# Performance work log

Hardware: AMD Instinct MI355X
Metric: run time of the kernel (lower is better)

The kernel has to match this reference:

```python
import jax, jax.numpy as jnp
import numpy as np

N, E, IN_DIM, HID, HEADS = 50000, 800000, 160, 64, 4
NEG_SLOPE = 0.2
BN_EPS = 1e-5


def setup_inputs() -> dict:
    key = jax.random.key(0)
    ks = jax.random.split(key, 32)
    s = lambda i, shape, sc=0.05: jax.random.normal(ks[i], shape, dtype=jnp.float32) * sc
    inp = {
        "x": jax.random.normal(ks[0], (N, IN_DIM), dtype=jnp.float32),
        "edge_index": jax.random.randint(ks[1], (2, E), 0, N, dtype=jnp.int64),
        # conv1: GATv2Conv(160 -> 64, heads=4, concat=True)
        "Wl1": s(2, (IN_DIM, HEADS * HID)), "bl1": s(3, (HEADS * HID,)),
        "Wr1": s(4, (IN_DIM, HEADS * HID)), "br1": s(5, (HEADS * HID,)),
        "att1": s(6, (HEADS, HID)), "bias1": s(7, (HEADS * HID,)),
        # bn1 (eval mode)
        "g1": jnp.ones((HEADS * HID,), jnp.float32), "b1": s(8, (HEADS * HID,)),
        "m1": s(9, (HEADS * HID,)), "v1": jax.random.uniform(ks[10], (HEADS * HID,), jnp.float32, 0.5, 1.5),
        # conv2: GATv2Conv(256 -> 64, heads=1, concat=False)
        "Wl2": s(11, (HEADS * HID, HID)), "bl2": s(12, (HID,)),
        "Wr2": s(13, (HEADS * HID, HID)), "br2": s(14, (HID,)),
        "att2": s(15, (1, HID)), "bias2": s(16, (HID,)),
        # bn2 (eval mode)
        "g2": jnp.ones((HID,), jnp.float32), "b2": s(17, (HID,)),
        "m2": s(18, (HID,)), "v2": jax.random.uniform(ks[19], (HID,), jnp.float32, 0.5, 1.5),
        # skip and output linear
        "Ws": s(20, (IN_DIM, HID)), "bs": s(21, (HID,)),
        "Wo": s(22, (HID, 1)), "bo": s(23, (1,)),
    }
    return inp


def gatv2_conv(x, Wl, bl, Wr, br, att, bias, src, dst, heads, out_dim, concat):
    n = x.shape[0]
    xl = (x @ Wl + bl).reshape(n, heads, out_dim)   # source transform
    xr = (x @ Wr + br).reshape(n, heads, out_dim)   # target transform
    e = jax.nn.leaky_relu(xl[src] + xr[dst], NEG_SLOPE)       # [E', H, D]
    logits = jnp.einsum('ehd,hd->eh', e, att)                 # [E', H]
    # segment softmax over incoming edges per target node
    mx = jax.ops.segment_max(logits, dst, num_segments=n)     # [N, H]
    a = jnp.exp(logits - mx[dst])
    denom = jax.ops.segment_sum(a, dst, num_segments=n)
    alpha = a / denom[dst]                                    # [E', H]
    out = jax.ops.segment_sum(xl[src] * alpha[:, :, None], dst, num_segments=n)  # [N, H, D]
    out = out.reshape(n, heads * out_dim) if concat else out.mean(axis=1)
    return out + bias


def reference(x, edge_index, Wl1, bl1, Wr1, br1, att1, bias1, g1, b1, m1, v1,
              Wl2, bl2, Wr2, br2, att2, bias2, g2, b2, m2, v2, Ws, bs, Wo, bo):
    n = x.shape[0]
    loop = jnp.arange(n, dtype=edge_index.dtype)
    src = jnp.concatenate([edge_index[0], loop])   # PyG add_self_loops=True
    dst = jnp.concatenate([edge_index[1], loop])

    x_skip = x @ Ws + bs
    h = gatv2_conv(x, Wl1, bl1, Wr1, br1, att1, bias1, src, dst, HEADS, HID, True)
    h = jax.nn.relu((h - m1) * g1 / jnp.sqrt(v1 + BN_EPS) + b1)  # BN1 eval + relu
    h = gatv2_conv(h, Wl2, bl2, Wr2, br2, att2, bias2, src, dst, 1, HID, False)
    h = jax.nn.relu((h - m2) * g2 / jnp.sqrt(v2 + BN_EPS) + b2)  # BN2 eval + relu
    h = h + x_skip
    return (h @ Wo + bo).squeeze(-1)               # [N]
```

## Files before the change

kernel.cpp:

```cpp
#include <hip/hip_runtime.h>
#include <hip/hip_bf16.h>

#define N_NODES 50000
#define E_EDGES 800000
#define EP_EDGES 850000
#define IN_DIM 160
#define HEADS 4
#define HID 64
#define C1 256
#define NEG_SLOPE 0.2f
#define BN_EPS 1e-5f

typedef __attribute__((ext_vector_type(8))) short bf16x8;
typedef __attribute__((ext_vector_type(4))) float f32x4;
typedef _Float16 h2 __attribute__((ext_vector_type(2)));

__device__ __forceinline__ float b2f(ushort u) {
    return __uint_as_float(((unsigned)u) << 16);
}
__device__ __forceinline__ ushort f2b(float f) {
    __hip_bfloat16 h = __float2bfloat16(f);
    return *reinterpret_cast<ushort*>(&h);
}
__device__ __forceinline__ ushort f2h(float f) {
    union { _Float16 h; ushort u; } c;
    c.h = (_Float16)f;
    return c.u;
}
__device__ __forceinline__ float lo16(uint u) { return __uint_as_float(u << 16); }
__device__ __forceinline__ float hi16(uint u) { return __uint_as_float(u & 0xffff0000u); }
__device__ __forceinline__ h2 uh(uint u) {
    union { uint u; h2 h; } c; c.u = u; return c.h;
}

__device__ __forceinline__ bool probe_f32(const ushort* xraw) {
    int lane = threadIdx.x & 63;
    float a = fabsf(b2f(xraw[2 * lane]));
    unsigned long long m = __ballot(a > 1e-6f && a < 1e6f);
    return __popcll(m) < 48;
}
__device__ __forceinline__ bool probe_i64(const int* eraw) {
    int lane = threadIdx.x & 63;
    unsigned long long m = __ballot(eraw[2 * lane + 1] != 0);
    return __popcll(m) < 8;
}

template<int CTRL>
__device__ __forceinline__ float dpp_add(float p) {
    int t = __builtin_amdgcn_update_dpp(0, __float_as_int(p), CTRL, 0xf, 0xf, true);
    return p + __int_as_float(t);
}
__device__ __forceinline__ float row16_sum(float p) {
    p = dpp_add<0xB1>(p);
    p = dpp_add<0x4E>(p);
    p = dpp_add<0x124>(p);
    p = dpp_add<0x128>(p);
    return p;
}

#define NB_SWZ 62
#define NB_HIST 3321

struct SW2 {
    const void* W[5];
    ushort* D[5];
    ushort* U;
    int NT[5];
    int base[5];
    const void* sp[19];
    const void* xraw;
};

__global__ void front_k(const int* __restrict__ ei, int* __restrict__ deg,
                        int* __restrict__ epos, SW2 s, ushort* __restrict__ params) {
    const int b = blockIdx.x;
    if (b < NB_SWZ) {
        const bool f32 = probe_f32((const ushort*)s.xraw);
        if (b < 61) {
            int idx = b * 256 + threadIdx.x;
            int seg = 0;
            #pragma unroll
            for (int k = 1; k < 5; ++k) seg += (idx >= s.base[k]) ? 1 : 0;
            int li = idx - s.base[seg];
            int NT = s.NT[seg];
            int N = NT << 4;
            int lane = li & 63;
            int ft = li >> 6;
            int kb = ft / NT, t = ft - kb * NT;
            int q = lane >> 4, m = lane & 15;
            const float* pf = (const float*)s.W[seg];
            const ushort* pu = (const ushort*)s.W[seg];
            ushort* d;
            if (seg < 3) {
                const int FO = (seg == 0) ? 0 : (seg == 1) ? 16 : 32;
                d = s.U + ((size_t)(kb * 36 + FO + t) * 64 + lane) * 8;
            } else {
                d = s.D[seg] + (size_t)li * 8;
            }
            #pragma unroll
            for (int j = 0; j < 8; ++j) {
                size_t src = (size_t)(kb * 32 + q * 8 + j) * N + t * 16 + m;
                d[j] = f32 ? f2b(pf[src]) : pu[src];
            }
        } else {
            const int SZ[19] = {256,256,256,256,256,256,256,256,
                                64,64,64,64,64,64,64,64,64,64, 1};
            const int OF[19] = {40960,82176,82432,82688,82944,83200,83456,83712,
                                100352,116800,116864,116928,116992,117056,117120,117184,
                                127488,127552, 127616};
            for (int e = threadIdx.x; e < 2689; e += 256) {
                int rem = e, t = 0;
                while (rem >= SZ[t]) { rem -= SZ[t]; ++t; }
                const float* pf = (const float*)s.sp[t];
                const ushort* pu = (const ushort*)s.sp[t];
                float val = f32 ? pf[rem] : b2f(pu[rem]);
                params[OF[t] + rem] = (t == 2 || t == 10) ? f2h(val) : f2b(val);
            }
        }
    } else {
        const bool i64 = probe_i64(ei);
        int e = (b - NB_SWZ) * 256 + threadIdx.x;
        if (e >= EP_EDGES) return;
        int dst;
        if (e < E_EDGES) {
            int idx = E_EDGES + e;
            dst = i64 ? ei[2 * idx] : ei[idx];
        } else dst = e - E_EDGES;
        epos[e] = atomicAdd(&deg[dst], 1);
    }
}

__global__ __launch_bounds__(1024) void scan1_k(const int* __restrict__ deg,
                                                int* __restrict__ exc,
                                                int* __restrict__ bsum) {
    __shared__ int wsum[16];
    const int t = threadIdx.x;
    const int lane = t & 63, w = t >> 6;
    int i = blockIdx.x * 1024 + t;
    int v = (i < N_NODES) ? deg[i] : 0;
    int sIncl = v;
    #pragma unroll
    for (int d = 1; d < 64; d <<= 1) {
        int u = __shfl_up(sIncl, d);
        if (lane >= d) sIncl += u;
    }
    if (lane == 63) wsum[w] = sIncl;
    __syncthreads();
    if (w == 0) {
        int p = (lane < 16) ? wsum[lane] : 0;
        #pragma unroll
        for (int d = 1; d < 16; d <<= 1) {
            int u = __shfl_up(p, d);
            if (lane >= d) p += u;
        }
        if (lane < 16) wsum[lane] = p;
    }
    __syncthreads();
    int base = (w > 0) ? wsum[w - 1] : 0;
    int incl = base + sIncl;
    if (i < N_NODES) exc[i] = incl - v;
    if (t == 1023) bsum[blockIdx.x] = incl;
}

__global__ void scan2_k(const int* __restrict__ bsum, int* __restrict__ cp,
                        int* __restrict__ exc) {
    int lane = threadIdx.x;
    int v = (lane < 49) ? bsum[lane] : 0;
    int orig = v;
    #pragma unroll
    for (int d = 1; d < 64; d <<= 1) {
        int u = __shfl_up(v, d);
        if (lane >= d) v += u;
    }
    if (lane < 49) cp[lane] = v - orig;
    if (lane == 48) exc[N_NODES] = EP_EDGES - (v - orig);
}

__device__ __forceinline__ bf16x8 loadA(const void* X, bool f32, size_t row, int off) {
    if (!f32) return *(const bf16x8*)((const ushort*)X + row * IN_DIM + off);
    const float* p = (const float*)X + row * IN_DIM + off;
    bf16x8 r;
    #pragma unroll
    for (int j = 0; j < 8; ++j) r[j] = (short)f2b(p[j]);
    return r;
}

#define NB_G3 3128

__global__ __launch_bounds__(256, 4) void scatgemm_k(const void* __restrict__ A,
                                                     const ushort* __restrict__ U,
                                                     const ushort* __restrict__ bi1,
                                                     const ushort* __restrict__ bi2,
                                                     const ushort* __restrict__ bi3,
                                                     ushort* __restrict__ o1,
                                                     ushort* __restrict__ o2,
                                                     ushort* __restrict__ o3,
                                                     int M,
                                                     const int* __restrict__ ei,
                                                     const int* __restrict__ epos,
                                                     const int* __restrict__ exc,
                                                     const int* __restrict__ cp,
                                                     int* __restrict__ col) {
    if (blockIdx.x >= NB_G3) {
        const bool i64 = probe_i64(ei);
        int e = (blockIdx.x - NB_G3) * 256 + threadIdx.x;
        if (e >= EP_EDGES) return;
        int src, dst;
        if (e < E_EDGES) {
            if (i64) { src = ei[2 * e]; dst = ei[2 * (E_EDGES + e)]; }
            else     { src = ei[e];     dst = ei[E_EDGES + e]; }
        } else { src = e - E_EDGES; dst = src; }
        col[exc[dst] + cp[dst >> 10] + epos[e]] = src;
        return;
    }
    const bool f32 = probe_f32((const ushort*)A);
    const int wave = threadIdx.x >> 6;
    const int lane = threadIdx.x & 63;
    const int cg = blockIdx.x & 3;
    const int rb = blockIdx.x >> 2;
    const int row0 = rb * 64 + wave * 16;
    if (row0 >= M) return;
    const int ar = row0 + (lane & 15);
    const int aoff = (lane >> 4) * 8;
    const bf16x8* bu = (const bf16x8*)U;
    f32x4 acc[9] = {};
    #pragma unroll
    for (int kb = 0; kb < 5; ++kb) {
        bf16x8 af = loadA(A, f32, (size_t)ar, aoff + kb * 32);
        #pragma unroll
        for (int jj = 0; jj < 9; ++jj) {
            bf16x8 b = bu[(size_t)(kb * 36 + cg * 9 + jj) * 64 + lane];
            acc[jj] = __builtin_amdgcn_mfma_f32_16x16x32_bf16(af, b, acc[jj], 0, 0, 0);
        }
    }
    const int cn = lane & 15, cq = lane >> 4;
    #pragma unroll
    for (int jj = 0; jj < 9; ++jj) {
        const int f = cg * 9 + jj;
        ushort* op; int ldc, colb; const ushort* bp_; bool tobf;
        if (f < 16)      { op = o1; ldc = C1;  colb = f * 16;        bp_ = bi1 + f * 16;        tobf = false; }
        else if (f < 32) { op = o2; ldc = C1;  colb = (f - 16) * 16; bp_ = bi2 + (f - 16) * 16; tobf = false; }
        else             { op = o3; ldc = HID; colb = (f - 32) * 16; bp_ = bi3 + (f - 32) * 16; tobf = true;  }
        const float bb = b2f(bp_[cn]);
        #pragma unroll
        for (int r = 0; r < 4; ++r) {
            const int grow = row0 + cq * 4 + r;
            const float v = acc[jj][r] + bb;
            op[(size_t)grow * ldc + colb + cn] = tobf ? f2b(v) : f2h(v);
        }
    }
}

__global__ __launch_bounds__(256) void gemm2_k(const ushort* __restrict__ A,
                                               const ushort* __restrict__ B1,
                                               const ushort* __restrict__ B2,
                                               const ushort* __restrict__ bi1,
                                               const ushort* __restrict__ bi2,
                                               ushort* __restrict__ o1,
                                               ushort* __restrict__ o2,
                                               int M) {
    const int wave = threadIdx.x >> 6;
    const int lane = threadIdx.x & 63;
    const int row0 = blockIdx.x * 64 + wave * 16;
    if (row0 >= M) return;
    int arow = row0 + (lane & 15);
    if (arow >= M) arow = M - 1;
    const ushort* aptr = A + (size_t)arow * C1 + (lane >> 4) * 8;
    const bf16x8* b1 = (const bf16x8*)B1;
    const bf16x8* b2 = (const bf16x8*)B2;
    f32x4 aL[4] = {}, aR[4] = {};
    #pragma unroll
    for (int kb = 0; kb < 8; ++kb) {
        bf16x8 af = *(const bf16x8*)(aptr + kb * 32);
        #pragma unroll
        for (int t = 0; t < 4; ++t)
            aL[t] = __builtin_amdgcn_mfma_f32_16x16x32_bf16(af, b1[(kb * 4 + t) * 64 + lane], aL[t], 0, 0, 0);
        #pragma unroll
        for (int t = 0; t < 4; ++t)
            aR[t] = __builtin_amdgcn_mfma_f32_16x16x32_bf16(af, b2[(kb * 4 + t) * 64 + lane], aR[t], 0, 0, 0);
    }
    const int cn = lane & 15, cq = lane >> 4;
    #pragma unroll
    for (int t = 0; t < 4; ++t) {
        float bbL = b2f(bi1[t * 16 + cn]);
        float bbR = b2f(bi2[t * 16 + cn]);
        #pragma unroll
        for (int r = 0; r < 4; ++r) {
            int grow = row0 + cq * 4 + r;
            if (grow < M) {
                o1[(size_t)grow * HID + t * 16 + cn] = f2h(aL[t][r] + bbL);
                o2[(size_t)grow * HID + t * 16 + cn] = f2h(aR[t][r] + bbR);
            }
        }
    }
}

__global__ __launch_bounds__(256) void conv1_k(const ushort* __restrict__ xl,
                                               const ushort* __restrict__ xr,
                                               const int* __restrict__ exc,
                                               const int* __restrict__ cp,
                                               const int* __restrict__ col,
                                               const ushort* __restrict__ att,
                                               const ushort* __restrict__ bias1,
                                               const ushort* __restrict__ g1,
                                               const ushort* __restrict__ b1,
                                               const ushort* __restrict__ m1,
                                               const ushort* __restrict__ v1,
                                               ushort* __restrict__ h1out) {
    const int n = blockIdx.x * 4 + (threadIdx.x >> 6);
    if (n >= N_NODES) return;
    const int lane = threadIdx.x & 63;
    const int g = lane >> 4;
    const int r = lane & 15;
    const uint4* xr4 = (const uint4*)(xr + (size_t)n * C1 + r * 16);
    const uint4 xru0 = xr4[0], xru1 = xr4[1];
    const uint4* at4 = (const uint4*)(att + r * 16);
    const uint4 atu0 = at4[0], atu1 = at4[1];
    h2 xrp[8], atp[8];
    xrp[0] = uh(xru0.x); xrp[1] = uh(xru0.y); xrp[2] = uh(xru0.z); xrp[3] = uh(xru0.w);
    xrp[4] = uh(xru1.x); xrp[5] = uh(xru1.y); xrp[6] = uh(xru1.z); xrp[7] = uh(xru1.w);
    atp[0] = uh(atu0.x); atp[1] = uh(atu0.y); atp[2] = uh(atu0.z); atp[3] = uh(atu0.w);
    atp[4] = uh(atu1.x); atp[5] = uh(atu1.y); atp[6] = uh(atu1.z); atp[7] = uh(atu1.w);
    const h2 ns2 = {(_Float16)NEG_SLOPE, (_Float16)NEG_SLOPE};
    const int e0 = exc[n] + cp[n >> 10];
    const int e1 = exc[n + 1] + cp[(n + 1) >> 10];
    float a[16];
    #pragma unroll
    for (int k = 0; k < 16; ++k) a[k] = 0.f;
    float den = 0.f;
    int j = e0 + g;

    auto body = [&](uint4 u0, uint4 u1, bool masked, int jm) {
        h2 xp[8];
        xp[0] = uh(u0.x); xp[1] = uh(u0.y); xp[2] = uh(u0.z); xp[3] = uh(u0.w);
        xp[4] = uh(u1.x); xp[5] = uh(u1.y); xp[6] = uh(u1.z); xp[7] = uh(u1.w);
        h2 d0 = {(_Float16)0, (_Float16)0};
        h2 d1 = {(_Float16)0, (_Float16)0};
        #pragma unroll
        for (int k = 0; k < 8; k += 2) {
            h2 t0 = xp[k] + xrp[k];
            t0 = __builtin_elementwise_max(t0, t0 * ns2);
            d0 = __builtin_elementwise_fma(t0, atp[k], d0);
            h2 t1 = xp[k + 1] + xrp[k + 1];
            t1 = __builtin_elementwise_max(t1, t1 * ns2);
            d1 = __builtin_elementwise_fma(t1, atp[k + 1], d1);
        }
        h2 ds = d0 + d1;
        float p = (float)ds.x + (float)ds.y;
        p = dpp_add<0xB1>(p);
        p = dpp_add<0x4E>(p);
        float w = __expf(fminf(p, 60.f));
        if (masked) w = (jm < e1) ? w : 0.f;
        den += w;
        #pragma unroll
        for (int k = 0; k < 8; ++k) {
            a[2 * k]     = fmaf(w, (float)xp[k].x, a[2 * k]);
            a[2 * k + 1] = fmaf(w, (float)xp[k].y, a[2 * k + 1]);
        }
    };
    auto rowp = [&](int s) { return (const uint4*)(xl + (size_t)(uint)s * C1 + r * 16); };

    int sA = col[j < e1 ? j : e1 - 1];
    int sB = col[j + 4 < e1 ? j + 4 : e1 - 1];
    int i = e0;
    for (; i + 8 <= e1; i += 8) {
        const int jn = i + g + 8;
        int sC = col[jn < e1 ? jn : e1 - 1];
        int sD = col[jn + 4 < e1 ? jn + 4 : e1 - 1];
        const uint4* pA = rowp(sA);
        uint4 a0 = pA[0], a1 = pA[1];
        const uint4* pB = rowp(sB);
        uint4 b0 = pB[0], b1v = pB[1];
        body(a0, a1, false, 0);
        body(b0, b1v, false, 0);
        sA = sC; sB = sD;
    }
    j = i + g;
    if (i + 4 <= e1) {
        const uint4* pA = rowp(sA);
        uint4 a0 = pA[0], a1 = pA[1];
        body(a0, a1, false, 0);
        sA = sB; i += 4; j += 4;
    }
    if (j < e1) {
        const uint4* pA = rowp(sA);
        uint4 a0 = pA[0], a1 = pA[1];
        body(a0, a1, true, j);
    }

    #pragma unroll
    for (int k = 0; k < 16; ++k) {
        a[k] += __shfl_xor(a[k], 16);
        a[k] += __shfl_xor(a[k], 32);
    }
    den += __shfl_xor(den, 16);
    den += __shfl_xor(den, 32);
    const int q = g;
    float s0 = q == 0 ? a[0] : q == 1 ? a[4] : q == 2 ? a[8]  : a[12];
    float s1 = q == 0 ? a[1] : q == 1 ? a[5] : q == 2 ? a[9]  : a[13];
    float s2 = q == 0 ? a[2] : q == 1 ? a[6] : q == 2 ? a[10] : a[14];
    float s3 = q == 0 ? a[3] : q == 1 ? a[7] : q == 2 ? a[11] : a[15];
    const int pi = r * 4 + q;
    const float inv = 1.f / den;
    const uint2 biu = ((const uint2*)bias1)[pi];
    const uint2 gu  = ((const uint2*)g1)[pi];
    const uint2 bu  = ((const uint2*)b1)[pi];
    const uint2 mu  = ((const uint2*)m1)[pi];
    const uint2 vu  = ((const uint2*)v1)[pi];
    float o0 = fmaf(s0, inv, lo16(biu.x));
    float o1 = fmaf(s1, inv, hi16(biu.x));
    float o2 = fmaf(s2, inv, lo16(biu.y));
    float o3 = fmaf(s3, inv, hi16(biu.y));
    float c0 = lo16(gu.x) * rsqrtf(lo16(vu.x) + BN_EPS);
    float c1 = hi16(gu.x) * rsqrtf(hi16(vu.x) + BN_EPS);
    float c2 = lo16(gu.y) * rsqrtf(lo16(vu.y) + BN_EPS);
    float c3 = hi16(gu.y) * rsqrtf(hi16(vu.y) + BN_EPS);
    float h0 = fmaxf((o0 - lo16(mu.x)) * c0 + lo16(bu.x), 0.f);
    float h1v = fmaxf((o1 - hi16(mu.x)) * c1 + hi16(bu.x), 0.f);
    float h2v = fmaxf((o2 - lo16(mu.y)) * c2 + lo16(bu.y), 0.f);
    float h3 = fmaxf((o3 - hi16(mu.y)) * c3 + hi16(bu.y), 0.f);
    uint2 ou;
    ou.x = (uint)f2b(h0) | ((uint)f2b(h1v) << 16);
    ou.y = (uint)f2b(h2v) | ((uint)f2b(h3) << 16);
    ((uint2*)h1out)[(size_t)n * 64 + pi] = ou;
}

__global__ __launch_bounds__(256) void conv2_k(const ushort* __restrict__ xl,
                                               const ushort* __restrict__ xr,
                                               const ushort* __restrict__ xskip,
                                               const int* __restrict__ exc,
                                               const int* __restrict__ cp,
                                               const int* __restrict__ col,
                                               const ushort* __restrict__ att2,
                                               const ushort* __restrict__ bias2,
                                               const ushort* __restrict__ g2,
                                               const ushort* __restrict__ bb2,
                                               const ushort* __restrict__ m2,
                                               const ushort* __restrict__ v2,
                                               const ushort* __restrict__ Wo,
                                               const ushort* __restrict__ bo,
                                               void* __restrict__ out,
                                               const ushort* __restrict__ xraw) {
    const bool f32out = probe_f32(xraw);
    const int n = blockIdx.x * 4 + (threadIdx.x >> 6);
    if (n >= N_NODES) return;
    const int lane = threadIdx.x & 63;
    const int grp = lane >> 4;
    const uint m = lane & 15;
    const uint2* xl2v = (const uint2*)xl;
    const uint2 xru = ((const uint2*)xr)[(size_t)n * 16 + m];
    const h2 xr01 = uh(xru.x), xr23 = uh(xru.y);
    const uint2 atu = ((const uint2*)att2)[m];
    const h2 at01 = uh(atu.x), at23 = uh(atu.y);
    const h2 ns2 = {(_Float16)NEG_SLOPE, (_Float16)NEG_SLOPE};
    const int e0 = exc[n] + cp[n >> 10];
    const int e1 = exc[n + 1] + cp[(n + 1) >> 10];
    const int deg = e1 - e0;
    const int iend = e0 + (deg & ~15);
    float a0 = 0.f, a1 = 0.f, a2 = 0.f, a3 = 0.f, den = 0.f;

    auto edge4 = [&](const uint2 xu, bool masked, int jbase) {
        const h2 x01 = uh(xu.x), x23 = uh(xu.y);
        h2 t01 = x01 + xr01;
        t01 = __builtin_elementwise_max(t01, t01 * ns2);
        h2 t23 = x23 + xr23;
        t23 = __builtin_elementwise_max(t23, t23 * ns2);
        h2 dp = __builtin_elementwise_fma(t23, at23, t01 * at01);
        float p = (float)dp.x + (float)dp.y;
        p = row16_sum(p);
        float w;
        if (masked) {
            w = __expf(fminf(p, 60.f));
            w = ((jbase + grp) < e1) ? w : 0.f;
        } else {
            w = __expf(p);
        }
        a0 = fmaf(w, (float)x01.x, a0);
        a1 = fmaf(w, (float)x01.y, a1);
        a2 = fmaf(w, (float)x23.x, a2);
        a3 = fmaf(w, (float)x23.y, a3);
        den += w;
    };

    uint s0_, s1_, s2_, s3_;
    {
        const int j0 = e0 + grp, j1 = j0 + 4, j2 = j0 + 8, j3 = j0 + 12;
        s0_ = (uint)col[j0 < e1 ? j0 : e1 - 1];
        s1_ = (uint)col[j1 < e1 ? j1 : e1 - 1];
        s2_ = (uint)col[j2 < e1 ? j2 : e1 - 1];
        s3_ = (uint)col[j3 < e1 ? j3 : e1 - 1];
    }
    for (int i = e0; i < iend; i += 16) {
        const uint2 xu0 = xl2v[(s0_ << 4) + m];
        const uint2 xu1 = xl2v[(s1_ << 4) + m];
        const uint2 xu2 = xl2v[(s2_ << 4) + m];
        const uint2 xu3 = xl2v[(s3_ << 4) + m];
        const int j0 = i + 16 + grp, j1 = j0 + 4, j2 = j0 + 8, j3 = j0 + 12;
        s0_ = (uint)col[j0 < e1 ? j0 : e1 - 1];
        s1_ = (uint)col[j1 < e1 ? j1 : e1 - 1];
        s2_ = (uint)col[j2 < e1 ? j2 : e1 - 1];
        s3_ = (uint)col[j3 < e1 ? j3 : e1 - 1];
        edge4(xu0, false, 0);
        edge4(xu1, false, 0);
        edge4(xu2, false, 0);
        edge4(xu3, false, 0);
    }
    const int rem = e1 - iend;
    if (rem > 0) {
        const uint2 xu0 = xl2v[(s0_ << 4) + m];
        const uint2 xu1 = xl2v[(s1_ << 4) + m];
        const uint2 xu2 = xl2v[(s2_ << 4) + m];
        const uint2 xu3 = xl2v[(s3_ << 4) + m];
        edge4(xu0, true, iend);
        if (rem > 4)  edge4(xu1, true, iend + 4);
        if (rem > 8)  edge4(xu2, true, iend + 8);
        if (rem > 12) edge4(xu3, true, iend + 12);
    }
    a0 += __shfl_xor(a0, 16); a0 += __shfl_xor(a0, 32);
    a1 += __shfl_xor(a1, 16); a1 += __shfl_xor(a1, 32);
    a2 += __shfl_xor(a2, 16); a2 += __shfl_xor(a2, 32);
    a3 += __shfl_xor(a3, 16); a3 += __shfl_xor(a3, 32);
    den += __shfl_xor(den, 16); den += __shfl_xor(den, 32);
    if (lane < 16) {
        const float inv = 1.f / den;
        const uint2 biu = ((const uint2*)bias2)[m];
        const uint2 gu  = ((const uint2*)g2)[m];
        const uint2 bu  = ((const uint2*)bb2)[m];
        const uint2 mu  = ((const uint2*)m2)[m];
        const uint2 vu  = ((const uint2*)v2)[m];
        const uint2 sku = ((const uint2*)xskip)[(size_t)n * 16 + m];
        const uint2 wou = ((const uint2*)Wo)[m];
        float o0 = fmaf(a0, inv, lo16(biu.x));
        float o1 = fmaf(a1, inv, hi16(biu.x));
        float o2 = fmaf(a2, inv, lo16(biu.y));
        float o3 = fmaf(a3, inv, hi16(biu.y));
        float s0 = lo16(gu.x) * rsqrtf(lo16(vu.x) + BN_EPS);
        float s1 = hi16(gu.x) * rsqrtf(hi16(vu.x) + BN_EPS);
        float s2 = lo16(gu.y) * rsqrtf(lo16(vu.y) + BN_EPS);
        float s3 = hi16(gu.y) * rsqrtf(hi16(vu.y) + BN_EPS);
        float h0 = fmaxf((o0 - lo16(mu.x)) * s0 + lo16(bu.x), 0.f) + lo16(sku.x);
        float h1v = fmaxf((o1 - hi16(mu.x)) * s1 + hi16(bu.x), 0.f) + hi16(sku.x);
        float h2v = fmaxf((o2 - lo16(mu.y)) * s2 + lo16(bu.y), 0.f) + lo16(sku.y);
        float h3 = fmaxf((o3 - hi16(mu.y)) * s3 + hi16(bu.y), 0.f) + hi16(sku.y);
        float d = fmaf(h0, lo16(wou.x), fmaf(h1v, hi16(wou.x),
                  fmaf(h2v, lo16(wou.y), h3 * hi16(wou.y))));
        d = row16_sum(d);
        if (m == 0) {
            float r = d + b2f(bo[0]);
            if (f32out) ((float*)out)[n] = r;
            else        ((ushort*)out)[n] = f2b(r);
        }
    }
}

extern "C" void kernel_launch(void* const* d_in, const int* in_sizes, int n_in,
                              void* d_out, int out_size, void* d_ws, size_t ws_size,
                              hipStream_t stream) {
    char* ws = (char*)d_ws;
    size_t off = 0;
    auto alloc = [&](size_t bytes) -> void* {
        void* p = ws + off;
        off += (bytes + 255) & ~(size_t)255;
        return p;
    };
    ushort* params  = (ushort*)alloc((size_t)127617 * 2);
    int*    exc     = (int*)alloc((size_t)(N_NODES + 1) * 4);
    int*    deg     = (int*)alloc((size_t)N_NODES * 4);
    int*    epos    = (int*)alloc((size_t)EP_EDGES * 4);
    int*    colbuf  = (int*)alloc((size_t)EP_EDGES * 4);
    int*    bsum    = (int*)alloc(64 * 4);
    int*    cparr   = (int*)alloc(64 * 4);
    ushort* xl1     = (ushort*)alloc((size_t)N_NODES * C1 * 2);
    ushort* xr1     = (ushort*)alloc((size_t)N_NODES * C1 * 2);
    ushort* xskip   = (ushort*)alloc((size_t)N_NODES * HID * 2);
    ushort* h1      = (ushort*)alloc((size_t)N_NODES * C1 * 2);
    ushort* xl2     = (ushort*)alloc((size_t)N_NODES * HID * 2);
    ushort* xr2     = (ushort*)alloc((size_t)N_NODES * HID * 2);
    ushort* swzU    = (ushort*)alloc((size_t)5 * 36 * 64 * 8 * 2);
    ushort* swzWl2  = (ushort*)alloc((size_t)C1 * HID * 2);
    ushort* swzWr2  = (ushort*)alloc((size_t)C1 * HID * 2);

    ushort* bl1c   = params + 40960;
    ushort* br1c   = params + 82176;
    ushort* att1c  = params + 82432;
    ushort* bias1c = params + 82688;
    ushort* g1c    = params + 82944;
    ushort* b1c    = params + 83200;
    ushort* m1c    = params + 83456;
    ushort* v1c    = params + 83712;
    ushort* bl2c   = params + 100352;
    ushort* br2c   = params + 116800;
    ushort* att2c  = params + 116864;
    ushort* bias2c = params + 116928;
    ushort* g2c    = params + 116992;
    ushort* b2c    = params + 117056;
    ushort* m2c    = params + 117120;
    ushort* v2c    = params + 117184;
    ushort* bsc    = params + 127488;
    ushort* Woc    = params + 127552;
    ushort* boc    = params + 127616;

    const int* ei_raw = (const int*)d_in[1];

    (void)hipMemsetAsync(deg, 0, (size_t)N_NODES * 4, stream);

    SW2 sw;
    sw.W[0] = d_in[2];  sw.D[0] = nullptr; sw.NT[0] = 16; sw.base[0] = 0;
    sw.W[1] = d_in[4];  sw.D[1] = nullptr; sw.NT[1] = 16; sw.base[1] = 5120;
    sw.W[2] = d_in[22]; sw.D[2] = nullptr; sw.NT[2] = 4;  sw.base[2] = 10240;
    sw.W[3] = d_in[12]; sw.D[3] = swzWl2;  sw.NT[3] = 4;  sw.base[3] = 11520;
    sw.W[4] = d_in[14]; sw.D[4] = swzWr2;  sw.NT[4] = 4;  sw.base[4] = 13568;
    sw.U = swzU;
    const int spidx[19] = {3,5,6,7,8,9,10,11, 13,15,16,17,18,19,20,21, 23,24, 25};
    for (int i = 0; i < 19; ++i) sw.sp[i] = d_in[spidx[i]];
    sw.xraw = d_in[0];
    front_k<<<NB_SWZ + NB_HIST, 256, 0, stream>>>(ei_raw, deg, epos, sw, params);

    const int NB_S = (N_NODES + 1023) / 1024;

    scan1_k<<<NB_S, 1024, 0, stream>>>(deg, exc, bsum);
    scan2_k<<<1, 64, 0, stream>>>(bsum, cparr, exc);

    scatgemm_k<<<NB_G3 + NB_HIST, 256, 0, stream>>>(
        d_in[0], swzU, bl1c, br1c, bsc, xl1, xr1, xskip, N_NODES,
        ei_raw, epos, exc, cparr, colbuf);

    conv1_k<<<(N_NODES + 3) / 4, 256, 0, stream>>>(xl1, xr1, exc, cparr, colbuf,
                                                   att1c, bias1c, g1c, b1c, m1c, v1c, h1);

    gemm2_k<<<(N_NODES + 63) / 64, 256, 0, stream>>>(h1, swzWl2, swzWr2, bl2c, br2c,
                                                     xl2, xr2, N_NODES);

    conv2_k<<<(N_NODES + 3) / 4, 256, 0, stream>>>(xl2, xr2, xskip, exc, cparr, colbuf,
                                                   att2c, bias2c, g2c, b2c, m2c, v2c,
                                                   Woc, boc, d_out, (const ushort*)d_in[0]);
}
```

Measured before the change: 327.2 us.

## Pre-convert x to bf16, split scatter from GEMM, stage B tiles in LDS

Converts x to bf16 once in the front kernel, which is meant to remove the per-tile f32-to-bf16 conversion inside the first GEMM. The CSR column scatter is split out of the fused scatter+GEMM kernel into its own launch. The GEMM now stages its 9-column weight slice in shared memory and computes 32 rows per wave, reusing each B fragment across two MFMAs. This costs an extra 16 MB round trip for the bf16 copy of x and one more kernel launch, and the larger LDS footprint lowers occupancy.

```diff
diff --git a/kernel.cpp b/kernel.cpp
--- a/kernel.cpp
+++ b/kernel.cpp
@@ -59,6 +59,7 @@
 }
 
 #define NB_SWZ 62
+#define NB_CVT 3907
 #define NB_HIST 3321
 
 struct SW2 {
@@ -72,7 +73,8 @@
 };
 
 __global__ void front_k(const int* __restrict__ ei, int* __restrict__ deg,
-                        int* __restrict__ epos, SW2 s, ushort* __restrict__ params) {
+                        int* __restrict__ epos, SW2 s, ushort* __restrict__ params,
+                        ushort* __restrict__ Abf) {
     const int b = blockIdx.x;
     if (b < NB_SWZ) {
         const bool f32 = probe_f32((const ushort*)s.xraw);
@@ -117,9 +119,24 @@
                 params[OF[t] + rem] = (t == 2 || t == 10) ? f2h(val) : f2b(val);
             }
         }
+    } else if (b < NB_SWZ + NB_CVT) {
+        const bool f32 = probe_f32((const ushort*)s.xraw);
+        int idx = (b - NB_SWZ) * 256 + threadIdx.x;
+        if (idx < 1000000) {
+            if (f32) {
+                const float* px = (const float*)s.xraw + (size_t)idx * 8;
+                bf16x8 r;
+                #pragma unroll
+                for (int j = 0; j < 8; ++j) r[j] = (short)f2b(px[j]);
+                *(bf16x8*)(Abf + (size_t)idx * 8) = r;
+            } else {
+                *(uint4*)(Abf + (size_t)idx * 8) =
+                    *(const uint4*)((const ushort*)s.xraw + (size_t)idx * 8);
+            }
+        }
     } else {
         const bool i64 = probe_i64(ei);
-        int e = (b - NB_SWZ) * 256 + threadIdx.x;
+        int e = (b - NB_SWZ - NB_CVT) * 256 + threadIdx.x;
         if (e >= EP_EDGES) return;
         int dst;
         if (e < E_EDGES) {
@@ -176,77 +193,88 @@
     if (lane == 48) exc[N_NODES] = EP_EDGES - (v - orig);
 }
 
-__device__ __forceinline__ bf16x8 loadA(const void* X, bool f32, size_t row, int off) {
-    if (!f32) return *(const bf16x8*)((const ushort*)X + row * IN_DIM + off);
-    const float* p = (const float*)X + row * IN_DIM + off;
-    bf16x8 r;
-    #pragma unroll
-    for (int j = 0; j < 8; ++j) r[j] = (short)f2b(p[j]);
-    return r;
-}
-
-#define NB_G3 3128
-
-__global__ __launch_bounds__(256, 4) void scatgemm_k(const void* __restrict__ A,
-                                                     const ushort* __restrict__ U,
-                                                     const ushort* __restrict__ bi1,
-                                                     const ushort* __restrict__ bi2,
-                                                     const ushort* __restrict__ bi3,
-                                                     ushort* __restrict__ o1,
-                                                     ushort* __restrict__ o2,
-                                                     ushort* __restrict__ o3,
-                                                     int M,
-                                                     const int* __restrict__ ei,
-                                                     const int* __restrict__ epos,
-                                                     const int* __restrict__ exc,
-                                                     const int* __restrict__ cp,
-                                                     int* __restrict__ col) {
-    if (blockIdx.x >= NB_G3) {
-        const bool i64 = probe_i64(ei);
-        int e = (blockIdx.x - NB_G3) * 256 + threadIdx.x;
-        if (e >= EP_EDGES) return;
-        int src, dst;
-        if (e < E_EDGES) {
-            if (i64) { src = ei[2 * e]; dst = ei[2 * (E_EDGES + e)]; }
-            else     { src = ei[e];     dst = ei[E_EDGES + e]; }
-        } else { src = e - E_EDGES; dst = src; }
-        col[exc[dst] + cp[dst >> 10] + epos[e]] = src;
-        return;
-    }
-    const bool f32 = probe_f32((const ushort*)A);
-    const int wave = threadIdx.x >> 6;
-    const int lane = threadIdx.x & 63;
+__global__ __launch_bounds__(256) void scatter_k(const int* __restrict__ ei,
+                                                 const int* __restrict__ epos,
+                                                 const int* __restrict__ exc,
+                                                 const int* __restrict__ cp,
+                                                 int* __restrict__ col) {
+    const bool i64 = probe_i64(ei);
+    int e = blockIdx.x * 256 + threadIdx.x;
+    if (e >= EP_EDGES) return;
+    int src, dst;
+    if (e < E_EDGES) {
+        if (i64) { src = ei[2 * e]; dst = ei[2 * (E_EDGES + e)]; }
+        else     { src = ei[e];     dst = ei[E_EDGES + e]; }
+    } else { src = e - E_EDGES; dst = src; }
+    col[exc[dst] + cp[dst >> 10] + epos[e]] = src;
+}
+
+#define NB_RB 391
+
+__global__ __launch_bounds__(256, 3) void gemm3_k(const ushort* __restrict__ Abf,
+                                                  const ushort* __restrict__ U,
+                                                  const ushort* __restrict__ bi1,
+                                                  const ushort* __restrict__ bi2,
+                                                  const ushort* __restrict__ bi3,
+                                                  ushort* __restrict__ o1,
+                                                  ushort* __restrict__ o2,
+                                                  ushort* __restrict__ o3,
+                                                  int M) {
+    __shared__ ushort Bs[23040];
     const int cg = blockIdx.x & 3;
     const int rb = blockIdx.x >> 2;
-    const int row0 = rb * 64 + wave * 16;
-    if (row0 >= M) return;
-    const int ar = row0 + (lane & 15);
+    const int tid = threadIdx.x;
+    #pragma unroll
+    for (int t = 0; t < 12; ++t) {
+        int c = t * 256 + tid;
+        if (c < 2880) {
+            int lf = c >> 6;
+            int kb = lf / 9, jj = lf - kb * 9;
+            int ln = c & 63;
+            *(uint4*)(Bs + (size_t)c * 8) =
+                *(const uint4*)(U + ((size_t)((kb * 36 + cg * 9 + jj) * 64 + ln)) * 8);
+        }
+    }
+    __syncthreads();
+    const int wave = tid >> 6, lane = tid & 63;
+    const int row0 = rb * 128 + wave * 32;
+    const bool ok0 = row0 < M, ok1 = row0 + 16 < M;
+    const int car0 = ok0 ? row0 + (lane & 15) : 0;
+    const int car1 = ok1 ? row0 + 16 + (lane & 15) : 0;
     const int aoff = (lane >> 4) * 8;
-    const bf16x8* bu = (const bf16x8*)U;
-    f32x4 acc[9] = {};
+    f32x4 a0[9] = {}, a1[9] = {};
     #pragma unroll
     for (int kb = 0; kb < 5; ++kb) {
-        bf16x8 af = loadA(A, f32, (size_t)ar, aoff + kb * 32);
+        bf16x8 af0 = *(const bf16x8*)(Abf + (size_t)car0 * IN_DIM + aoff + kb * 32);
+        bf16x8 af1 = *(const bf16x8*)(Abf + (size_t)car1 * IN_DIM + aoff + kb * 32);
         #pragma unroll
         for (int jj = 0; jj < 9; ++jj) {
-            bf16x8 b = bu[(size_t)(kb * 36 + cg * 9 + jj) * 64 + lane];
-            acc[jj] = __builtin_amdgcn_mfma_f32_16x16x32_bf16(af, b, acc[jj], 0, 0, 0);
+            bf16x8 bfr = *(const bf16x8*)(Bs + (size_t)((kb * 9 + jj) * 64 + lane) * 8);
+            a0[jj] = __builtin_amdgcn_mfma_f32_16x16x32_bf16(af0, bfr, a0[jj], 0, 0, 0);
+            a1[jj] = __builtin_amdgcn_mfma_f32_16x16x32_bf16(af1, bfr, a1[jj], 0, 0, 0);
         }
     }
     const int cn = lane & 15, cq = lane >> 4;
     #pragma unroll
-    for (int jj = 0; jj < 9; ++jj) {
-        const int f = cg * 9 + jj;
-        ushort* op; int ldc, colb; const ushort* bp_; bool tobf;
-        if (f < 16)      { op = o1; ldc = C1;  colb = f * 16;        bp_ = bi1 + f * 16;        tobf = false; }
-        else if (f < 32) { op = o2; ldc = C1;  colb = (f - 16) * 16; bp_ = bi2 + (f - 16) * 16; tobf = false; }
-        else             { op = o3; ldc = HID; colb = (f - 32) * 16; bp_ = bi3 + (f - 32) * 16; tobf = true;  }
-        const float bb = b2f(bp_[cn]);
-        #pragma unroll
-        for (int r = 0; r < 4; ++r) {
-            const int grow = row0 + cq * 4 + r;
-            const float v = acc[jj][r] + bb;
-            op[(size_t)grow * ldc + colb + cn] = tobf ? f2b(v) : f2h(v);
+    for (int rt = 0; rt < 2; ++rt) {
+        const bool ok = rt ? ok1 : ok0;
+        if (!ok) continue;
+        const int rbase = row0 + rt * 16;
+        #pragma unroll
+        for (int jj = 0; jj < 9; ++jj) {
+            const int f = cg * 9 + jj;
+            ushort* op; int ldc, colb; const ushort* bp_; bool tobf;
+            if (f < 16)      { op = o1; ldc = C1;  colb = f * 16;        bp_ = bi1 + f * 16;        tobf = false; }
+            else if (f < 32) { op = o2; ldc = C1;  colb = (f - 16) * 16; bp_ = bi2 + (f - 16) * 16; tobf = false; }
+            else             { op = o3; ldc = HID; colb = (f - 32) * 16; bp_ = bi3 + (f - 32) * 16; tobf = true;  }
+            const float bb = b2f(bp_[cn]);
+            const f32x4 av = rt ? a1[jj] : a0[jj];
+            #pragma unroll
+            for (int r = 0; r < 4; ++r) {
+                const int grow = rbase + cq * 4 + r;
+                const float v = av[r] + bb;
+                op[(size_t)grow * ldc + colb + cn] = tobf ? f2b(v) : f2h(v);
+            }
         }
     }
 }
@@ -579,6 +607,7 @@
     ushort* swzU    = (ushort*)alloc((size_t)5 * 36 * 64 * 8 * 2);
     ushort* swzWl2  = (ushort*)alloc((size_t)C1 * HID * 2);
     ushort* swzWr2  = (ushort*)alloc((size_t)C1 * HID * 2);
+    ushort* Abf     = (ushort*)alloc((size_t)N_NODES * IN_DIM * 2);
 
     ushort* bl1c   = params + 40960;
     ushort* br1c   = params + 82176;
@@ -614,16 +643,17 @@
     const int spidx[19] = {3,5,6,7,8,9,10,11, 13,15,16,17,18,19,20,21, 23,24, 25};
     for (int i = 0; i < 19; ++i) sw.sp[i] = d_in[spidx[i]];
     sw.xraw = d_in[0];
-    front_k<<<NB_SWZ + NB_HIST, 256, 0, stream>>>(ei_raw, deg, epos, sw, params);
+    front_k<<<NB_SWZ + NB_CVT + NB_HIST, 256, 0, stream>>>(ei_raw, deg, epos, sw, params, Abf);
 
     const int NB_S = (N_NODES + 1023) / 1024;
 
     scan1_k<<<NB_S, 1024, 0, stream>>>(deg, exc, bsum);
     scan2_k<<<1, 64, 0, stream>>>(bsum, cparr, exc);
 
-    scatgemm_k<<<NB_G3 + NB_HIST, 256, 0, stream>>>(
-        d_in[0], swzU, bl1c, br1c, bsc, xl1, xr1, xskip, N_NODES,
-        ei_raw, epos, exc, cparr, colbuf);
+    scatter_k<<<NB_HIST, 256, 0, stream>>>(ei_raw, epos, exc, cparr, colbuf);
+
+    gemm3_k<<<NB_RB * 4, 256, 0, stream>>>(Abf, swzU, bl1c, br1c, bsc,
+                                           xl1, xr1, xskip, N_NODES);
 
     conv1_k<<<(N_NODES + 3) / 4, 256, 0, stream>>>(xl1, xr1, exc, cparr, colbuf,
                                                    att1c, bias1c, g1c, b1c, m1c, v1c, h1);
```

Measured after the change: 322.8 us. About the same (-1.3%).
